# Optimization experiments

Hardware: AMD Instinct MI355X
Metric: run time of the kernel (lower is better)

The kernel has to match this reference:

```python
import jax, jax.numpy as jnp
import numpy as np

B, N, C_IN, C_OUT, CHEB_K, EMBED = 64, 2048, 64, 64, 3, 16

def setup_inputs() -> dict:
    key = jax.random.key(0)
    k1, k2, k3, k4 = jax.random.split(key, 4)
    x = jax.random.normal(k1, (B, N, C_IN), dtype=jnp.float32)
    node_embedding = jax.random.normal(k2, (N, EMBED), dtype=jnp.float32)
    weights_pool = jax.random.normal(k3, (EMBED, CHEB_K, C_IN, C_OUT), dtype=jnp.float32) * 0.1
    bias_pool = jax.random.normal(k4, (EMBED, C_OUT), dtype=jnp.float32) * 0.1
    return {"x": x, "node_embedding": node_embedding,
            "weights_pool": weights_pool, "bias_pool": bias_pool}

def reference(x, node_embedding, weights_pool, bias_pool):
    cheb_k = weights_pool.shape[1]
    n = node_embedding.shape[0]
    # adaptive adjacency: softmax over rows of relu(E @ E^T)
    support = jax.nn.softmax(jax.nn.relu(node_embedding @ node_embedding.T), axis=1)
    # Chebyshev recursion: T0 = I, T1 = support, Tk = 2*support@Tk-1 - Tk-2
    supports = [jnp.eye(n, dtype=support.dtype), support]
    for _ in range(2, cheb_k):
        supports.append(2.0 * support @ supports[-1] - supports[-2])
    supports = jnp.stack(supports, axis=0)  # (K, N, N)
    # per-node weights/bias generated from embedding
    weights = jnp.einsum('nd,dkio->nkio', node_embedding, weights_pool)  # (N,K,Cin,Cout)
    bias = node_embedding @ bias_pool  # (N, Cout)
    # graph conv: gather K-hop features then per-node grouped matmul
    x_g = jnp.einsum('knm,bmc->bnkc', supports, x)  # (B,N,K,Cin)
    x_gconv = jnp.einsum('bnki,nkio->bno', x_g, weights) + bias
    return x_gconv
```

## Files before the change

kernel.cpp:

```cpp
#include <hip/hip_runtime.h>
#include <math.h>

#define NN    2048
#define BATCH 64
#define CIN   64
#define COUT  64
#define EMB   16
#define JDIM  4096
#define WKI   192

typedef __bf16 bf16_t;
typedef __bf16 bf16x8 __attribute__((ext_vector_type(8)));
typedef float  f32x4  __attribute__((ext_vector_type(4)));
typedef unsigned int u32x2 __attribute__((ext_vector_type(2)));
typedef unsigned int u32x4 __attribute__((ext_vector_type(4)));

#define GLOAD16(gp, lp) __builtin_amdgcn_global_load_lds( \
    (const __attribute__((address_space(1))) void*)(gp),  \
    (__attribute__((address_space(3))) void*)(lp), 16, 0, 0)

static __device__ __forceinline__ unsigned short bfbits(float f) {
    return __builtin_bit_cast(unsigned short, (bf16_t)f);
}

__global__ __launch_bounds__(256) void prelude_kernel(
    const float* __restrict__ x,  const float* __restrict__ E,
    const float* __restrict__ wp, bf16_t* __restrict__ Y0,
    bf16_t* __restrict__ Sb,      bf16_t* __restrict__ Wt) {
    __shared__ float smem[64 * 65];
    const int bid = blockIdx.x;
    const int tid = threadIdx.x;

    if (bid < 768) {
        float (*sE)[16] = reinterpret_cast<float(*)[16]>(smem);
        const int n0   = (bid / 12) * 32;
        const int oki0 = (bid % 12) * 1024 + 4 * tid;
        const int o = oki0 / WKI, r0 = oki0 % WKI;

        if (tid < 128) {
            const int node = tid >> 2, q = tid & 3;
            *reinterpret_cast<float4*>(&sE[node][q * 4]) =
                *reinterpret_cast<const float4*>(E + (size_t)(n0 + node) * EMB + q * 4);
        }
        float w[4][EMB];
#pragma unroll
        for (int d = 0; d < EMB; ++d)
#pragma unroll
            for (int j = 0; j < 4; ++j)
                w[j][d] = wp[(size_t)(d * WKI + r0 + j) * 64 + o];
        __syncthreads();

#pragma unroll 2
        for (int nn = 0; nn < 32; ++nn) {
            float4 e0 = *reinterpret_cast<const float4*>(&sE[nn][0]);
            float4 e1 = *reinterpret_cast<const float4*>(&sE[nn][4]);
            float4 e2 = *reinterpret_cast<const float4*>(&sE[nn][8]);
            float4 e3 = *reinterpret_cast<const float4*>(&sE[nn][12]);
            float en[EMB] = {e0.x,e0.y,e0.z,e0.w, e1.x,e1.y,e1.z,e1.w,
                             e2.x,e2.y,e2.z,e2.w, e3.x,e3.y,e3.z,e3.w};
            float a[4] = {};
#pragma unroll
            for (int d = 0; d < EMB; ++d)
#pragma unroll
                for (int j = 0; j < 4; ++j) a[j] += en[d] * w[j][d];
            ushort4 pk;
            pk.x = bfbits(a[0]); pk.y = bfbits(a[1]);
            pk.z = bfbits(a[2]); pk.w = bfbits(a[3]);
            __builtin_nontemporal_store(
                __builtin_bit_cast(u32x2, pk),
                reinterpret_cast<u32x2*>(Wt + (size_t)(n0 + nn) * 12288 + oki0));
        }
    } else if (bid < 2816) {
        float* vals = smem;
        float* red  = smem + 2048;
        const int n = bid - 768;

        float en[EMB];
#pragma unroll
        for (int d = 0; d < EMB; ++d) en[d] = E[n * EMB + d];

        float lmax = -1e30f;
        for (int m = tid; m < NN; m += 256) {
            const float4* em = reinterpret_cast<const float4*>(E + m * EMB);
            float dot = 0.f;
#pragma unroll
            for (int q = 0; q < EMB / 4; ++q) {
                float4 v = em[q];
                dot += en[q*4+0]*v.x + en[q*4+1]*v.y + en[q*4+2]*v.z + en[q*4+3]*v.w;
            }
            float r = fmaxf(dot, 0.f);
            vals[m] = r;
            lmax = fmaxf(lmax, r);
        }
#pragma unroll
        for (int off = 32; off > 0; off >>= 1)
            lmax = fmaxf(lmax, __shfl_down(lmax, off, 64));
        if ((tid & 63) == 0) red[tid >> 6] = lmax;
        __syncthreads();
        const float gmax = fmaxf(fmaxf(red[0], red[1]), fmaxf(red[2], red[3]));
        __syncthreads();

        float lsum = 0.f;
        for (int m = tid; m < NN; m += 256) {
            float e = expf(vals[m] - gmax);
            vals[m] = e;
            lsum += e;
        }
#pragma unroll
        for (int off = 32; off > 0; off >>= 1)
            lsum += __shfl_down(lsum, off, 64);
        if ((tid & 63) == 0) red[tid >> 6] = lsum;
        __syncthreads();
        const float inv = 1.f / (red[0] + red[1] + red[2] + red[3]);

        for (int m = tid; m < NN; m += 256)
            Sb[(size_t)n * NN + m] = (bf16_t)(vals[m] * inv);
    } else {
        float (*tile)[65] = reinterpret_cast<float(*)[65]>(smem);
        const int yb = bid - 2816;
        const int n0 = (yb & 31) * 64, b = yb >> 5;
        const int c = tid & 63, nn0 = tid >> 6;
        const float* src = x + ((size_t)b * NN + n0) * CIN + c;
#pragma unroll
        for (int p = 0; p < 16; ++p) {
            int nn = nn0 + p * 4;
            tile[nn][c] = src[(size_t)nn * CIN];
        }
        __syncthreads();
        const int cc = tid >> 2, q = tid & 3;
        bf16_t* dst = Y0 + (size_t)(b * 64 + cc) * NN + n0 + q * 16;
#pragma unroll
        for (int s4 = 0; s4 < 4; ++s4) {
            ushort4 pk;
            pk.x = bfbits(tile[q * 16 + s4 * 4 + 0][cc]);
            pk.y = bfbits(tile[q * 16 + s4 * 4 + 1][cc]);
            pk.z = bfbits(tile[q * 16 + s4 * 4 + 2][cc]);
            pk.w = bfbits(tile[q * 16 + s4 * 4 + 3][cc]);
            *reinterpret_cast<ushort4*>(dst + s4 * 4) = pk;
        }
    }
}

template<int MODE>
__global__ __launch_bounds__(256) void gemm_bt(
    const bf16_t* __restrict__ A, const bf16_t* __restrict__ Bt,
    bf16_t* __restrict__ Cj, bf16_t* __restrict__ GT) {
    __shared__ bf16_t smem[128 * 136];
    bf16_t* As = smem;
    bf16_t* Bs = smem + 4096;
    bf16_t* T  = smem;
    const int tid  = threadIdx.x;
    const int wave = tid >> 6, lane = tid & 63;
    const int pBlk = blockIdx.x * 128;
    const int mBlk = blockIdx.y * 128;
    const int K = NN;

    const bf16_t* aSrc = A  + (size_t)(mBlk + wave * 32 + (lane >> 2)) * K + (lane & 3) * 8;
    const bf16_t* bSrc = Bt + (size_t)(pBlk + wave * 32 + (lane >> 2)) * K + (lane & 3) * 8;
    bf16_t* aDst = As + wave * 1024;
    bf16_t* bDst = Bs + wave * 1024;

    f32x4 acc[4][4] = {};
    const int wr = wave >> 1, wc = wave & 1;
    const int lrow = lane & 15, lk = (lane >> 4) * 8;

    for (int k0 = 0; k0 < K; k0 += 32) {
        GLOAD16(aSrc + k0,                  aDst);
        GLOAD16(aSrc + k0 + (size_t)16 * K, aDst + 512);
        GLOAD16(bSrc + k0,                  bDst);
        GLOAD16(bSrc + k0 + (size_t)16 * K, bDst + 512);
        __syncthreads();

        bf16x8 af[4], bb[4];
#pragma unroll
        for (int mf = 0; mf < 4; ++mf)
            af[mf] = *reinterpret_cast<const bf16x8*>(
                &As[(wr * 64 + mf * 16 + lrow) * 32 + lk]);
#pragma unroll
        for (int nf = 0; nf < 4; ++nf)
            bb[nf] = *reinterpret_cast<const bf16x8*>(
                &Bs[(wc * 64 + nf * 16 + lrow) * 32 + lk]);
#pragma unroll
        for (int mf = 0; mf < 4; ++mf)
#pragma unroll
            for (int nf = 0; nf < 4; ++nf)
                acc[mf][nf] = __builtin_amdgcn_mfma_f32_16x16x32_bf16(
                    af[mf], bb[nf], acc[mf][nf], 0, 0, 0);
        __syncthreads();
    }

    const int orow = (lane >> 4) * 4, ocol = lane & 15;
    if (MODE == 0) {
#pragma unroll
        for (int mf = 0; mf < 4; ++mf)
#pragma unroll
            for (int nf = 0; nf < 4; ++nf)
#pragma unroll
                for (int r = 0; r < 4; ++r) {
                    size_t row = (size_t)(mBlk + wr * 64 + mf * 16 + orow + r);
                    size_t col = (size_t)(pBlk + wc * 64 + nf * 16 + ocol);
                    Cj[row * NN + col] = (bf16_t)acc[mf][nf][r];
                }
    }
    const float scale = (MODE == 1) ? 2.f : 1.f;
#pragma unroll
    for (int mf = 0; mf < 4; ++mf)
#pragma unroll
        for (int nf = 0; nf < 4; ++nf)
#pragma unroll
            for (int r = 0; r < 4; ++r) {
                int trow = wr * 64 + mf * 16 + orow + r;
                int tcol = wc * 64 + nf * 16 + ocol;
                T[(size_t)tcol * 136 + trow] = (bf16_t)(scale * acc[mf][nf][r]);
            }
    __syncthreads();
    {
        const int row = tid >> 1, half = tid & 1;
        const bf16_t* src = T + (size_t)row * 136 + half * 64;
        bf16_t* dst = GT + (size_t)(pBlk + row) * JDIM + mBlk + half * 64;
#pragma unroll
        for (int s = 0; s < 8; ++s)
            *reinterpret_cast<uint4*>(dst + s * 8) =
                *reinterpret_cast<const uint4*>(src + s * 8);
    }
}

__global__ __launch_bounds__(256) void gconv_kernel(
    const float* __restrict__ x,   const float* __restrict__ E,
    const float* __restrict__ bp,  const bf16_t* __restrict__ G1T,
    const bf16_t* __restrict__ G2T, const bf16_t* __restrict__ Wt,
    float* __restrict__ out) {
    __shared__ bf16_t g[64][200];
    const int n = blockIdx.x;
    const int tid = threadIdx.x, wave = tid >> 6, lane = tid & 63;
    const int lrow = lane & 15, lk = (lane >> 4) * 8;
    const int o = wave * 16 + lrow;

    const bf16_t* wtn = Wt + (size_t)n * 12288 + (size_t)o * WKI;
    bf16x8 bb[6];
#pragma unroll
    for (int ks = 0; ks < 6; ++ks)
        bb[ks] = __builtin_bit_cast(bf16x8, __builtin_nontemporal_load(
            reinterpret_cast<const u32x4*>(wtn + ks * 32 + lk)));
    float bo = 0.f;
    {
        const float* en = E + (size_t)n * EMB;
#pragma unroll
        for (int d = 0; d < EMB; ++d) bo += en[d] * bp[d * COUT + o];
    }

#pragma unroll
    for (int p = 0; p < 2; ++p) {
        int idx = p * 256 + tid;
        int b = idx >> 3, ic = (idx & 7) * 8;
        const float4* xs = reinterpret_cast<const float4*>(
            x + ((size_t)b * NN + n) * CIN + ic);
        float4 x0 = xs[0], x1 = xs[1];
        uint4 g1v = *reinterpret_cast<const uint4*>(G1T + (size_t)n * JDIM + idx * 8);
        uint4 g2v = *reinterpret_cast<const uint4*>(G2T + (size_t)n * JDIM + idx * 8);
        float xv[8] = {x0.x, x0.y, x0.z, x0.w, x1.x, x1.y, x1.z, x1.w};
        const bf16_t* g2p = reinterpret_cast<const bf16_t*>(&g2v);
        ushort4 g0b[2], g2b[2];
#pragma unroll
        for (int e = 0; e < 8; ++e) {
            ((unsigned short*)g0b)[e] = bfbits(xv[e]);
            ((unsigned short*)g2b)[e] = bfbits((float)g2p[e] - xv[e]);
        }
        *reinterpret_cast<uint4*>(&g[b][ic])       = *reinterpret_cast<uint4*>(g0b);
        *reinterpret_cast<uint4*>(&g[b][64 + ic])  = g1v;
        *reinterpret_cast<uint4*>(&g[b][128 + ic]) = *reinterpret_cast<uint4*>(g2b);
    }
    __syncthreads();

    f32x4 acc[4] = {};
#pragma unroll
    for (int ks = 0; ks < 6; ++ks)
#pragma unroll
        for (int mf = 0; mf < 4; ++mf) {
            bf16x8 af = *reinterpret_cast<const bf16x8*>(&g[mf * 16 + lrow][ks * 32 + lk]);
            acc[mf] = __builtin_amdgcn_mfma_f32_16x16x32_bf16(af, bb[ks], acc[mf], 0, 0, 0);
        }
#pragma unroll
    for (int mf = 0; mf < 4; ++mf)
#pragma unroll
        for (int r = 0; r < 4; ++r) {
            int b = mf * 16 + (lane >> 4) * 4 + r;
            __builtin_nontemporal_store(acc[mf][r] + bo,
                &out[((size_t)b * NN + n) * COUT + o]);
        }
}

extern "C" void kernel_launch(void* const* d_in, const int* in_sizes, int n_in,
                              void* d_out, int out_size, void* d_ws, size_t ws_size,
                              hipStream_t stream) {
    const float* x  = (const float*)d_in[0];
    const float* E  = (const float*)d_in[1];
    const float* wp = (const float*)d_in[2];
    const float* bp = (const float*)d_in[3];
    float* out = (float*)d_out;

    bf16_t* ws = (bf16_t*)d_ws;
    bf16_t* Wt  = ws;
    bf16_t* Sb  = Wt + (size_t)NN * 12288;
    bf16_t* Y0  = Sb + (size_t)NN * NN;
    bf16_t* Y1  = Y0 + (size_t)JDIM * NN;
    bf16_t* G1T = Y1 + (size_t)JDIM * NN;
    bf16_t* G2T = Y0;

    prelude_kernel<<<768 + 2048 + 2048, 256, 0, stream>>>(x, E, wp, Y0, Sb, Wt);

    dim3 ggrid(NN / 128, JDIM / 128);
    gemm_bt<0><<<ggrid, 256, 0, stream>>>(Y0, Sb, Y1, G1T);
    gemm_bt<1><<<ggrid, 256, 0, stream>>>(Y1, Sb, nullptr, G2T);

    gconv_kernel<<<NN, 256, 0, stream>>>(x, E, bp, G1T, G2T, Wt, out);
}
```

Baseline: 264.1 us.

## Split weight generation into its own kernel with LDS-staged weight pool

Moves per-node weight generation out of the combined prelude kernel into a separate wgen kernel launched after the softmax/transpose kernel. The new kernel stages the needed weights_pool columns in shared memory with cooperative loads, replacing strided per-thread global loads. It also uses twice as many blocks, each thread producing two outputs instead of four. This is meant to cut uncoalesced global traffic and improve occupancy, at the cost of an extra kernel launch, a larger LDS footprint and narrower 4-byte stores.

Result: no change. 263.5 us (-0.2%).

```diff
diff --git a/kernel.cpp b/kernel.cpp
--- a/kernel.cpp
+++ b/kernel.cpp
@@ -12,7 +12,6 @@
 typedef __bf16 bf16_t;
 typedef __bf16 bf16x8 __attribute__((ext_vector_type(8)));
 typedef float  f32x4  __attribute__((ext_vector_type(4)));
-typedef unsigned int u32x2 __attribute__((ext_vector_type(2)));
 typedef unsigned int u32x4 __attribute__((ext_vector_type(4)));
 
 #define GLOAD16(gp, lp) __builtin_amdgcn_global_load_lds( \
@@ -23,57 +22,72 @@
     return __builtin_bit_cast(unsigned short, (bf16_t)f);
 }
 
-__global__ __launch_bounds__(256) void prelude_kernel(
-    const float* __restrict__ x,  const float* __restrict__ E,
-    const float* __restrict__ wp, bf16_t* __restrict__ Y0,
-    bf16_t* __restrict__ Sb,      bf16_t* __restrict__ Wt) {
+__global__ __launch_bounds__(256) void wgen_kernel(
+    const float* __restrict__ E, const float* __restrict__ wp,
+    bf16_t* __restrict__ Wt) {
+    __shared__ float wL[3072 * 4];
+    __shared__ float sE[32][16];
+    const int s  = blockIdx.x % 24;
+    const int n0 = (blockIdx.x / 24) * 32;
+    const int t  = threadIdx.x;
+    const int oki0 = s * 512 + 2 * t;
+    const int o = oki0 / WKI, r0 = oki0 % WKI;
+    const int o_lo = (s * 512) / WKI;
+
+    if (t < 128) {
+        const int node = t >> 2, q = t & 3;
+        *reinterpret_cast<float4*>(&sE[node][q * 4]) =
+            *reinterpret_cast<const float4*>(E + (size_t)(n0 + node) * EMB + q * 4);
+    }
+    {
+        const int oo  = t & 3;
+        const int col = min(o_lo + oo, 63);
+#pragma unroll
+        for (int i = 0; i < 48; ++i) {
+            int dr = (t >> 2) + i * 64;
+            wL[dr * 4 + oo] = wp[(size_t)dr * 64 + col];
+        }
+    }
+    __syncthreads();
+
+    float w[2][EMB];
+#pragma unroll
+    for (int d = 0; d < EMB; ++d) {
+        w[0][d] = wL[(d * WKI + r0) * 4 + (o - o_lo)];
+        w[1][d] = wL[(d * WKI + r0 + 1) * 4 + (o - o_lo)];
+    }
+
+#pragma unroll 2
+    for (int nn = 0; nn < 32; ++nn) {
+        float4 e0 = *reinterpret_cast<const float4*>(&sE[nn][0]);
+        float4 e1 = *reinterpret_cast<const float4*>(&sE[nn][4]);
+        float4 e2 = *reinterpret_cast<const float4*>(&sE[nn][8]);
+        float4 e3 = *reinterpret_cast<const float4*>(&sE[nn][12]);
+        float en[EMB] = {e0.x,e0.y,e0.z,e0.w, e1.x,e1.y,e1.z,e1.w,
+                         e2.x,e2.y,e2.z,e2.w, e3.x,e3.y,e3.z,e3.w};
+        float a0 = 0.f, a1 = 0.f;
+#pragma unroll
+        for (int d = 0; d < EMB; ++d) {
+            a0 += en[d] * w[0][d];
+            a1 += en[d] * w[1][d];
+        }
+        unsigned int pk = (unsigned int)bfbits(a0) | ((unsigned int)bfbits(a1) << 16);
+        __builtin_nontemporal_store(pk,
+            reinterpret_cast<unsigned int*>(Wt + (size_t)(n0 + nn) * 12288 + oki0));
+    }
+}
+
+__global__ __launch_bounds__(256) void sy_kernel(
+    const float* __restrict__ x, const float* __restrict__ E,
+    bf16_t* __restrict__ Y0, bf16_t* __restrict__ Sb) {
     __shared__ float smem[64 * 65];
     const int bid = blockIdx.x;
     const int tid = threadIdx.x;
 
-    if (bid < 768) {
-        float (*sE)[16] = reinterpret_cast<float(*)[16]>(smem);
-        const int n0   = (bid / 12) * 32;
-        const int oki0 = (bid % 12) * 1024 + 4 * tid;
-        const int o = oki0 / WKI, r0 = oki0 % WKI;
-
-        if (tid < 128) {
-            const int node = tid >> 2, q = tid & 3;
-            *reinterpret_cast<float4*>(&sE[node][q * 4]) =
-                *reinterpret_cast<const float4*>(E + (size_t)(n0 + node) * EMB + q * 4);
-        }
-        float w[4][EMB];
-#pragma unroll
-        for (int d = 0; d < EMB; ++d)
-#pragma unroll
-            for (int j = 0; j < 4; ++j)
-                w[j][d] = wp[(size_t)(d * WKI + r0 + j) * 64 + o];
-        __syncthreads();
-
-#pragma unroll 2
-        for (int nn = 0; nn < 32; ++nn) {
-            float4 e0 = *reinterpret_cast<const float4*>(&sE[nn][0]);
-            float4 e1 = *reinterpret_cast<const float4*>(&sE[nn][4]);
-            float4 e2 = *reinterpret_cast<const float4*>(&sE[nn][8]);
-            float4 e3 = *reinterpret_cast<const float4*>(&sE[nn][12]);
-            float en[EMB] = {e0.x,e0.y,e0.z,e0.w, e1.x,e1.y,e1.z,e1.w,
-                             e2.x,e2.y,e2.z,e2.w, e3.x,e3.y,e3.z,e3.w};
-            float a[4] = {};
-#pragma unroll
-            for (int d = 0; d < EMB; ++d)
-#pragma unroll
-                for (int j = 0; j < 4; ++j) a[j] += en[d] * w[j][d];
-            ushort4 pk;
-            pk.x = bfbits(a[0]); pk.y = bfbits(a[1]);
-            pk.z = bfbits(a[2]); pk.w = bfbits(a[3]);
-            __builtin_nontemporal_store(
-                __builtin_bit_cast(u32x2, pk),
-                reinterpret_cast<u32x2*>(Wt + (size_t)(n0 + nn) * 12288 + oki0));
-        }
-    } else if (bid < 2816) {
+    if (bid < 2048) {
         float* vals = smem;
         float* red  = smem + 2048;
-        const int n = bid - 768;
+        const int n = bid;
 
         float en[EMB];
 #pragma unroll
@@ -117,7 +131,7 @@
             Sb[(size_t)n * NN + m] = (bf16_t)(vals[m] * inv);
     } else {
         float (*tile)[65] = reinterpret_cast<float(*)[65]>(smem);
-        const int yb = bid - 2816;
+        const int yb = bid - 2048;
         const int n0 = (yb & 31) * 64, b = yb >> 5;
         const int c = tid & 63, nn0 = tid >> 6;
         const float* src = x + ((size_t)b * NN + n0) * CIN + c;
@@ -307,7 +321,8 @@
     bf16_t* G1T = Y1 + (size_t)JDIM * NN;
     bf16_t* G2T = Y0;
 
-    prelude_kernel<<<768 + 2048 + 2048, 256, 0, stream>>>(x, E, wp, Y0, Sb, Wt);
+    sy_kernel<<<4096, 256, 0, stream>>>(x, E, Y0, Sb);
+    wgen_kernel<<<24 * 64, 256, 0, stream>>>(E, wp, Wt);
 
     dim3 ggrid(NN / 128, JDIM / 128);
     gemm_bt<0><<<ggrid, 256, 0, stream>>>(Y0, Sb, Y1, G1T);
```
